# Performance work log

Hardware: AMD Instinct MI355X
Metric: run time of the kernel (lower is better)

Reference implementation:

```python
import jax, jax.numpy as jnp
import numpy as np

N_AGENTS = 32
UNIT_DIM = 64
HIDDEN = 128
BATCH = 1024
STATE_DIM = 128


def setup_inputs() -> dict:
    key = jax.random.key(0)
    ks = jax.random.split(key, 8)
    s = 0.05
    return {
        "state": jax.random.normal(ks[0], (BATCH, STATE_DIM), dtype=jnp.float32),
        "unit_states": jax.random.normal(ks[1], (N_AGENTS, BATCH, UNIT_DIM), dtype=jnp.float32),
        # edge_predictor params, stored [in, out] so y = x @ W + b (matches torch Linear math)
        "W1": jax.random.normal(ks[2], (2 * UNIT_DIM, HIDDEN), dtype=jnp.float32) * s,
        "b1": jnp.zeros((HIDDEN,), dtype=jnp.float32),
        "W2": jax.random.normal(ks[3], (HIDDEN, HIDDEN), dtype=jnp.float32) * s,
        "b2": jnp.zeros((HIDDEN,), dtype=jnp.float32),
        "W3": jax.random.normal(ks[4], (HIDDEN, 1), dtype=jnp.float32) * s,
        "b3": jnp.zeros((1,), dtype=jnp.float32),
    }


def reference(state, unit_states, W1, b1, W2, b2, W3, b3):
    # unit_states: [n_agents, B, d] -> [B, n_agents, d]  (permute(1,0,2))
    us = jnp.transpose(unit_states, (1, 0, 2))
    d = us.shape[-1]
    # Pairwise concat [us_i, us_j] through the first Linear is equivalent to
    # splitting W1 into its i-half and j-half and broadcast-adding (same math,
    # avoids materializing the [B,n,n,2d] concat tensor). Dropout rate is 0.0
    # (eval-mode identity).
    hi = us @ W1[:d]   # [B, n, H]
    hj = us @ W1[d:]   # [B, n, H]
    h = jax.nn.relu(hi[:, :, None, :] + hj[:, None, :, :] + b1)  # [B, n, n, H]
    h = jax.nn.relu(h @ W2 + b2)                                  # [B, n, n, H]
    logits = (h @ W3 + b3)[..., 0]                                # [B, n, n]
    adj = jax.nn.sigmoid(logits)
    # graph_add_self_loop = True
    adj = adj + jnp.eye(adj.shape[-1], dtype=adj.dtype)[None]
    return adj
```

## Files before the change

kernel.cpp:

```cpp
#include <hip/hip_runtime.h>
#include <hip/hip_bf16.h>

#define BATCH 1024
#define NA 32
#define UD 64
#define HID 128

typedef short bf16x8 __attribute__((ext_vector_type(8)));
typedef float f32x4 __attribute__((ext_vector_type(4)));

static __device__ __forceinline__ short f2bf(float x) {
    union { __hip_bfloat16 b; short s; } u;
    u.b = __float2bfloat16(x);
    return u.s;
}

__global__ void prep_weights(const float* __restrict__ W1,
                             const float* __restrict__ W2,
                             short* __restrict__ ws)
{
    int tid  = blockIdx.x * blockDim.x + threadIdx.x;
    int unit = tid >> 6;
    int lane = tid & 63;
    int l15  = lane & 15;
    int lq   = lane >> 4;
    bf16x8 v;
    if (unit < 32) {
        int ks = unit >> 3, nt = unit & 7;
        int col = nt * 16 + l15;
        int k0  = ks * 32 + lq * 8;
        #pragma unroll
        for (int e = 0; e < 8; ++e)
            v[e] = f2bf(W2[(k0 + e) * HID + col]);
    } else {
        int u = unit - 32;
        int h = u >> 4, ks = (u >> 3) & 1, nt = u & 7;
        int col = nt * 16 + l15;
        int k0  = ks * 32 + lq * 8;
        #pragma unroll
        for (int e = 0; e < 8; ++e)
            v[e] = f2bf(W1[(h * UD + k0 + e) * HID + col]);
    }
    *(bf16x8*)&ws[(size_t)(unit * 64 + lane) * 8] = v;
}

template <bool FROM_WS>
__global__ __launch_bounds__(512, 2)
void graph_learner_kernel(const float* __restrict__ us_g,
                          const float* __restrict__ W1,
                          const float* __restrict__ b1,
                          const float* __restrict__ W2,
                          const float* __restrict__ b2,
                          const float* __restrict__ W3,
                          const float* __restrict__ b3,
                          const short* __restrict__ ws,
                          float* __restrict__ out)
{
    __shared__ short us_bf[NA * UD] __attribute__((aligned(16)));
    __shared__ float hi_lds[NA * HID] __attribute__((aligned(16)));
    __shared__ float hj_lds[NA * HID] __attribute__((aligned(16)));

    const int b    = blockIdx.x;
    const int t    = threadIdx.x;
    const int w    = t >> 6;
    const int lane = t & 63;
    const int l15  = lane & 15;
    const int lq   = lane >> 4;

    {
        int i  = t >> 4;
        int d0 = (t & 15) * 4;
        const float* src = us_g + ((size_t)i * BATCH + (size_t)b) * UD + d0;
        float4 v = *(const float4*)src;
        int c  = d0 >> 3;
        int hs = (d0 >> 2) & 1;
        int idx = i * UD + (((c ^ (i & 7)) << 3) + (hs << 2));
        short4 s4;
        s4.x = f2bf(v.x); s4.y = f2bf(v.y); s4.z = f2bf(v.z); s4.w = f2bf(v.w);
        *(short4*)&us_bf[idx] = s4;
    }

    const int Mt  = w >> 2;
    const int nt0 = (w & 3) * 2;

    bf16x8 w1f[2][2][2];
    float  b1v[2];
    bf16x8 w2f[32];
    float  b2v[8], w3v[8];

    #pragma unroll
    for (int n = 0; n < 2; ++n)
        b1v[n] = b1[(nt0 + n) * 16 + l15];
    #pragma unroll
    for (int nt = 0; nt < 8; ++nt) {
        int col = nt * 16 + l15;
        b2v[nt] = b2[col];
        w3v[nt] = W3[col];
    }
    const float b3s = b3[0];

    if (FROM_WS) {
        #pragma unroll
        for (int i = 0; i < 32; ++i)
            w2f[i] = *(const bf16x8*)&ws[(size_t)(i * 64 + lane) * 8];
        #pragma unroll
        for (int n = 0; n < 2; ++n)
            #pragma unroll
            for (int h = 0; h < 2; ++h)
                #pragma unroll
                for (int ks = 0; ks < 2; ++ks) {
                    int u = h * 16 + ks * 8 + (nt0 + n);
                    w1f[n][h][ks] = *(const bf16x8*)&ws[(size_t)((32 + u) * 64 + lane) * 8];
                }
    } else {
        #pragma unroll
        for (int n = 0; n < 2; ++n) {
            int col = (nt0 + n) * 16 + l15;
            #pragma unroll
            for (int ks = 0; ks < 2; ++ks)
                #pragma unroll
                for (int e = 0; e < 8; ++e) {
                    int k = ks * 32 + lq * 8 + e;
                    w1f[n][0][ks][e] = f2bf(W1[k * HID + col]);
                    w1f[n][1][ks][e] = f2bf(W1[(UD + k) * HID + col]);
                }
        }
        #pragma unroll
        for (int ks = 0; ks < 4; ++ks)
            #pragma unroll
            for (int nt = 0; nt < 8; ++nt) {
                int col = nt * 16 + l15;
                int k0  = ks * 32 + lq * 8;
                #pragma unroll
                for (int e = 0; e < 8; ++e)
                    w2f[ks * 8 + nt][e] = f2bf(W2[(k0 + e) * HID + col]);
            }
    }

    __syncthreads();

    {
        const f32x4 zf = {0.f, 0.f, 0.f, 0.f};
        bf16x8 af[2];
        #pragma unroll
        for (int ks = 0; ks < 2; ++ks) {
            int row = Mt * 16 + l15;
            int c   = ks * 4 + lq;
            af[ks] = *(const bf16x8*)&us_bf[row * UD + ((c ^ (row & 7)) << 3)];
        }
        f32x4 ahi[2] = {zf, zf}, ahj[2] = {zf, zf};
        #pragma unroll
        for (int ks = 0; ks < 2; ++ks) {
            #pragma unroll
            for (int n = 0; n < 2; ++n) {
                ahi[n] = __builtin_amdgcn_mfma_f32_16x16x32_bf16(af[ks], w1f[n][0][ks], ahi[n], 0, 0, 0);
                ahj[n] = __builtin_amdgcn_mfma_f32_16x16x32_bf16(af[ks], w1f[n][1][ks], ahj[n], 0, 0, 0);
            }
        }
        #pragma unroll
        for (int n = 0; n < 2; ++n) {
            int col = (nt0 + n) * 16 + l15;
            #pragma unroll
            for (int r = 0; r < 4; ++r) {
                int rowi = Mt * 16 + lq * 4 + r;
                int idx  = rowi * HID + ((((col >> 2) ^ (rowi & 7)) << 2) + (col & 3));
                hi_lds[idx] = ahi[n][r] + b1v[n];
                hj_lds[idx] = ahj[n][r];
            }
        }
    }
    __syncthreads();

    #pragma unroll 1
    for (int mt = w; mt < 64; mt += 8) {
        const int i   = mt >> 1;
        const int j   = ((mt & 1) << 4) + l15;
        const float* hir = &hi_lds[i * HID];
        const float* hjr = &hj_lds[j * HID];
        const int isz = i & 7, jsz = j & 7;

        const f32x4 zf = {0.f, 0.f, 0.f, 0.f};
        f32x4 acc[8];
        #pragma unroll
        for (int nt = 0; nt < 8; ++nt) acc[nt] = zf;

        #pragma unroll
        for (int ks = 0; ks < 4; ++ks) {
            int c0 = ks * 8 + lq * 2;
            f32x4 h0 = *(const f32x4*)&hir[((c0    ) ^ isz) << 2];
            f32x4 h1 = *(const f32x4*)&hir[((c0 + 1) ^ isz) << 2];
            f32x4 g0 = *(const f32x4*)&hjr[((c0    ) ^ jsz) << 2];
            f32x4 g1 = *(const f32x4*)&hjr[((c0 + 1) ^ jsz) << 2];
            bf16x8 a;
            #pragma unroll
            for (int e = 0; e < 4; ++e) {
                a[e]     = f2bf(fmaxf(h0[e] + g0[e], 0.f));
                a[e + 4] = f2bf(fmaxf(h1[e] + g1[e], 0.f));
            }
            #pragma unroll
            for (int nt = 0; nt < 8; ++nt)
                acc[nt] = __builtin_amdgcn_mfma_f32_16x16x32_bf16(a, w2f[ks * 8 + nt], acc[nt], 0, 0, 0);
        }

        float p0r = 0.f, p1r = 0.f, p2r = 0.f, p3r = 0.f;
        #pragma unroll
        for (int nt = 0; nt < 8; ++nt) {
            p0r += fmaxf(acc[nt][0] + b2v[nt], 0.f) * w3v[nt];
            p1r += fmaxf(acc[nt][1] + b2v[nt], 0.f) * w3v[nt];
            p2r += fmaxf(acc[nt][2] + b2v[nt], 0.f) * w3v[nt];
            p3r += fmaxf(acc[nt][3] + b2v[nt], 0.f) * w3v[nt];
        }
        #pragma unroll
        for (int m = 1; m < 16; m <<= 1) {
            p0r += __shfl_xor(p0r, m);
            p1r += __shfl_xor(p1r, m);
            p2r += __shfl_xor(p2r, m);
            p3r += __shfl_xor(p3r, m);
        }
        if (l15 == 0) {
            int pbase = mt * 16 + lq * 4;
            float4 o;
            {
                float x = p0r + b3s; int p = pbase + 0;
                o.x = 1.f / (1.f + __expf(-x)) + (((p >> 5) == (p & 31)) ? 1.f : 0.f);
            }
            {
                float x = p1r + b3s; int p = pbase + 1;
                o.y = 1.f / (1.f + __expf(-x)) + (((p >> 5) == (p & 31)) ? 1.f : 0.f);
            }
            {
                float x = p2r + b3s; int p = pbase + 2;
                o.z = 1.f / (1.f + __expf(-x)) + (((p >> 5) == (p & 31)) ? 1.f : 0.f);
            }
            {
                float x = p3r + b3s; int p = pbase + 3;
                o.w = 1.f / (1.f + __expf(-x)) + (((p >> 5) == (p & 31)) ? 1.f : 0.f);
            }
            *(float4*)&out[(size_t)b * (NA * NA) + pbase] = o;
        }
    }
}

extern "C" void kernel_launch(void* const* d_in, const int* in_sizes, int n_in,
                              void* d_out, int out_size, void* d_ws, size_t ws_size,
                              hipStream_t stream) {
    const float* us = (const float*)d_in[1];
    const float* W1 = (const float*)d_in[2];
    const float* b1 = (const float*)d_in[3];
    const float* W2 = (const float*)d_in[4];
    const float* b2 = (const float*)d_in[5];
    const float* W3 = (const float*)d_in[6];
    const float* b3 = (const float*)d_in[7];
    float* out = (float*)d_out;
    short* ws  = (short*)d_ws;

    const bool use_ws = (ws_size >= 64u * 64u * 8u * sizeof(short));
    if (use_ws) {
        prep_weights<<<dim3(16), dim3(256), 0, stream>>>(W1, W2, ws);
        graph_learner_kernel<true><<<dim3(BATCH), dim3(512), 0, stream>>>(
            us, W1, b1, W2, b2, W3, b3, ws, out);
    } else {
        graph_learner_kernel<false><<<dim3(BATCH), dim3(512), 0, stream>>>(
            us, W1, b1, W2, b2, W3, b3, ws, out);
    }
}
```

Measured before the change: 136.2 us.

## Switch to fp16 MFMA with packed fp16 LDS, transposed layer-2 and 256-thread blocks

Replaces bf16 with fp16 for the weights, unit states and hidden activations. hi/hj are now kept as fp16 in LDS, so the pairwise add and ReLU run as packed half-precision vector ops instead of per-element fp32 math followed by a bf16 convert. The layer-2 MFMA operands are swapped, which puts the output features along lanes; the W3 reduction then needs only two shuffles, and biases are folded into the accumulator initial values. Blocks shrink to 256 threads (4 waves, 16 tiles each) and the W2 register load is deferred until after layer 1. This risks fp16 overflow or precision differences in the hidden sums, and it changes the occupancy balance.

```diff
diff --git a/kernel.cpp b/kernel.cpp
--- a/kernel.cpp
+++ b/kernel.cpp
@@ -6,32 +6,26 @@
 #define UD 64
 #define HID 128
 
-typedef short bf16x8 __attribute__((ext_vector_type(8)));
+typedef _Float16 f16x8 __attribute__((ext_vector_type(8)));
 typedef float f32x4 __attribute__((ext_vector_type(4)));
-
-static __device__ __forceinline__ short f2bf(float x) {
-    union { __hip_bfloat16 b; short s; } u;
-    u.b = __float2bfloat16(x);
-    return u.s;
-}
 
 __global__ void prep_weights(const float* __restrict__ W1,
                              const float* __restrict__ W2,
-                             short* __restrict__ ws)
+                             _Float16* __restrict__ ws)
 {
     int tid  = blockIdx.x * blockDim.x + threadIdx.x;
     int unit = tid >> 6;
     int lane = tid & 63;
     int l15  = lane & 15;
     int lq   = lane >> 4;
-    bf16x8 v;
+    f16x8 v;
     if (unit < 32) {
         int ks = unit >> 3, nt = unit & 7;
         int col = nt * 16 + l15;
         int k0  = ks * 32 + lq * 8;
         #pragma unroll
         for (int e = 0; e < 8; ++e)
-            v[e] = f2bf(W2[(k0 + e) * HID + col]);
+            v[e] = (_Float16)W2[(k0 + e) * HID + col];
     } else {
         int u = unit - 32;
         int h = u >> 4, ks = (u >> 3) & 1, nt = u & 7;
@@ -39,13 +33,13 @@
         int k0  = ks * 32 + lq * 8;
         #pragma unroll
         for (int e = 0; e < 8; ++e)
-            v[e] = f2bf(W1[(h * UD + k0 + e) * HID + col]);
-    }
-    *(bf16x8*)&ws[(size_t)(unit * 64 + lane) * 8] = v;
+            v[e] = (_Float16)W1[(h * UD + k0 + e) * HID + col];
+    }
+    *(f16x8*)&ws[(size_t)(unit * 64 + lane) * 8] = v;
 }
 
 template <bool FROM_WS>
-__global__ __launch_bounds__(512, 2)
+__global__ __launch_bounds__(256, 2)
 void graph_learner_kernel(const float* __restrict__ us_g,
                           const float* __restrict__ W1,
                           const float* __restrict__ b1,
@@ -53,12 +47,12 @@
                           const float* __restrict__ b2,
                           const float* __restrict__ W3,
                           const float* __restrict__ b3,
-                          const short* __restrict__ ws,
+                          const _Float16* __restrict__ ws,
                           float* __restrict__ out)
 {
-    __shared__ short us_bf[NA * UD] __attribute__((aligned(16)));
-    __shared__ float hi_lds[NA * HID] __attribute__((aligned(16)));
-    __shared__ float hj_lds[NA * HID] __attribute__((aligned(16)));
+    __shared__ _Float16 us_f16[NA * UD]  __attribute__((aligned(16)));
+    __shared__ _Float16 hi_lds[NA * HID] __attribute__((aligned(16)));
+    __shared__ _Float16 hj_lds[NA * HID] __attribute__((aligned(16)));
 
     const int b    = blockIdx.x;
     const int t    = threadIdx.x;
@@ -68,63 +62,93 @@
     const int lq   = lane >> 4;
 
     {
-        int i  = t >> 4;
-        int d0 = (t & 15) * 4;
-        const float* src = us_g + ((size_t)i * BATCH + (size_t)b) * UD + d0;
-        float4 v = *(const float4*)src;
-        int c  = d0 >> 3;
-        int hs = (d0 >> 2) & 1;
-        int idx = i * UD + (((c ^ (i & 7)) << 3) + (hs << 2));
-        short4 s4;
-        s4.x = f2bf(v.x); s4.y = f2bf(v.y); s4.z = f2bf(v.z); s4.w = f2bf(v.w);
-        *(short4*)&us_bf[idx] = s4;
-    }
-
-    const int Mt  = w >> 2;
-    const int nt0 = (w & 3) * 2;
-
-    bf16x8 w1f[2][2][2];
-    float  b1v[2];
-    bf16x8 w2f[32];
-    float  b2v[8], w3v[8];
-
-    #pragma unroll
-    for (int n = 0; n < 2; ++n)
-        b1v[n] = b1[(nt0 + n) * 16 + l15];
+        int i  = t >> 3;
+        int c  = t & 7;
+        const float* src = us_g + ((size_t)i * BATCH + (size_t)b) * UD + c * 8;
+        float4 va = *(const float4*)src;
+        float4 vb = *(const float4*)(src + 4);
+        f16x8 v8;
+        v8[0] = (_Float16)va.x; v8[1] = (_Float16)va.y;
+        v8[2] = (_Float16)va.z; v8[3] = (_Float16)va.w;
+        v8[4] = (_Float16)vb.x; v8[5] = (_Float16)vb.y;
+        v8[6] = (_Float16)vb.z; v8[7] = (_Float16)vb.w;
+        *(f16x8*)&us_f16[i * UD + ((c ^ (i & 7)) << 3)] = v8;
+    }
+
+    f32x4 b2q[8], w3q[8];
     #pragma unroll
     for (int nt = 0; nt < 8; ++nt) {
-        int col = nt * 16 + l15;
-        b2v[nt] = b2[col];
-        w3v[nt] = W3[col];
+        b2q[nt] = *(const f32x4*)&b2[nt * 16 + lq * 4];
+        w3q[nt] = *(const f32x4*)&W3[nt * 16 + lq * 4];
     }
     const float b3s = b3[0];
 
-    if (FROM_WS) {
-        #pragma unroll
-        for (int i = 0; i < 32; ++i)
-            w2f[i] = *(const bf16x8*)&ws[(size_t)(i * 64 + lane) * 8];
-        #pragma unroll
-        for (int n = 0; n < 2; ++n)
+    const int Mt = w >> 1;
+    const int nh = w & 1;
+
+    f16x8 w1f[4][2][2];
+    float b1v[4];
+    #pragma unroll
+    for (int n = 0; n < 4; ++n) {
+        int nt = nh * 4 + n;
+        b1v[n] = b1[nt * 16 + l15];
+        if (FROM_WS) {
             #pragma unroll
             for (int h = 0; h < 2; ++h)
                 #pragma unroll
                 for (int ks = 0; ks < 2; ++ks) {
-                    int u = h * 16 + ks * 8 + (nt0 + n);
-                    w1f[n][h][ks] = *(const bf16x8*)&ws[(size_t)((32 + u) * 64 + lane) * 8];
+                    int u = 32 + h * 16 + ks * 8 + nt;
+                    w1f[n][h][ks] = *(const f16x8*)&ws[(size_t)(u * 64 + lane) * 8];
                 }
+        } else {
+            int col = nt * 16 + l15;
+            #pragma unroll
+            for (int h = 0; h < 2; ++h)
+                #pragma unroll
+                for (int ks = 0; ks < 2; ++ks)
+                    #pragma unroll
+                    for (int e = 0; e < 8; ++e)
+                        w1f[n][h][ks][e] = (_Float16)W1[(h * UD + ks * 32 + lq * 8 + e) * HID + col];
+        }
+    }
+
+    __syncthreads();
+
+    {
+        f16x8 af[2];
+        #pragma unroll
+        for (int ks = 0; ks < 2; ++ks) {
+            int row = Mt * 16 + l15;
+            int c   = ks * 4 + lq;
+            af[ks] = *(const f16x8*)&us_f16[row * UD + ((c ^ (row & 7)) << 3)];
+        }
+        #pragma unroll
+        for (int n = 0; n < 4; ++n) {
+            int nt = nh * 4 + n;
+            f32x4 ahi = {b1v[n], b1v[n], b1v[n], b1v[n]};
+            f32x4 ahj = {0.f, 0.f, 0.f, 0.f};
+            #pragma unroll
+            for (int ks = 0; ks < 2; ++ks) {
+                ahi = __builtin_amdgcn_mfma_f32_16x16x32_f16(af[ks], w1f[n][0][ks], ahi, 0, 0, 0);
+                ahj = __builtin_amdgcn_mfma_f32_16x16x32_f16(af[ks], w1f[n][1][ks], ahj, 0, 0, 0);
+            }
+            #pragma unroll
+            for (int r = 0; r < 4; ++r) {
+                int row = Mt * 16 + lq * 4 + r;
+                int col = nt * 16 + l15;
+                int idx = row * HID + ((((col >> 3) ^ (row & 15)) << 3) + (col & 7));
+                hi_lds[idx] = (_Float16)ahi[r];
+                hj_lds[idx] = (_Float16)ahj[r];
+            }
+        }
+    }
+
+    f16x8 w2f[32];
+    if (FROM_WS) {
+        #pragma unroll
+        for (int q = 0; q < 32; ++q)
+            w2f[q] = *(const f16x8*)&ws[(size_t)(q * 64 + lane) * 8];
     } else {
-        #pragma unroll
-        for (int n = 0; n < 2; ++n) {
-            int col = (nt0 + n) * 16 + l15;
-            #pragma unroll
-            for (int ks = 0; ks < 2; ++ks)
-                #pragma unroll
-                for (int e = 0; e < 8; ++e) {
-                    int k = ks * 32 + lq * 8 + e;
-                    w1f[n][0][ks][e] = f2bf(W1[k * HID + col]);
-                    w1f[n][1][ks][e] = f2bf(W1[(UD + k) * HID + col]);
-                }
-        }
         #pragma unroll
         for (int ks = 0; ks < 4; ++ks)
             #pragma unroll
@@ -133,111 +157,59 @@
                 int k0  = ks * 32 + lq * 8;
                 #pragma unroll
                 for (int e = 0; e < 8; ++e)
-                    w2f[ks * 8 + nt][e] = f2bf(W2[(k0 + e) * HID + col]);
+                    w2f[ks * 8 + nt][e] = (_Float16)W2[(k0 + e) * HID + col];
             }
     }
 
     __syncthreads();
 
-    {
-        const f32x4 zf = {0.f, 0.f, 0.f, 0.f};
-        bf16x8 af[2];
-        #pragma unroll
-        for (int ks = 0; ks < 2; ++ks) {
-            int row = Mt * 16 + l15;
-            int c   = ks * 4 + lq;
-            af[ks] = *(const bf16x8*)&us_bf[row * UD + ((c ^ (row & 7)) << 3)];
-        }
-        f32x4 ahi[2] = {zf, zf}, ahj[2] = {zf, zf};
-        #pragma unroll
-        for (int ks = 0; ks < 2; ++ks) {
-            #pragma unroll
-            for (int n = 0; n < 2; ++n) {
-                ahi[n] = __builtin_amdgcn_mfma_f32_16x16x32_bf16(af[ks], w1f[n][0][ks], ahi[n], 0, 0, 0);
-                ahj[n] = __builtin_amdgcn_mfma_f32_16x16x32_bf16(af[ks], w1f[n][1][ks], ahj[n], 0, 0, 0);
-            }
-        }
-        #pragma unroll
-        for (int n = 0; n < 2; ++n) {
-            int col = (nt0 + n) * 16 + l15;
-            #pragma unroll
-            for (int r = 0; r < 4; ++r) {
-                int rowi = Mt * 16 + lq * 4 + r;
-                int idx  = rowi * HID + ((((col >> 2) ^ (rowi & 7)) << 2) + (col & 3));
-                hi_lds[idx] = ahi[n][r] + b1v[n];
-                hj_lds[idx] = ahj[n][r];
-            }
-        }
-    }
-    __syncthreads();
+    #pragma unroll
+    for (int q = 0; q < 32; q += 4)
+        asm volatile("" : "+v"(w2f[q]), "+v"(w2f[q + 1]), "+v"(w2f[q + 2]), "+v"(w2f[q + 3]));
 
     #pragma unroll 1
-    for (int mt = w; mt < 64; mt += 8) {
-        const int i   = mt >> 1;
-        const int j   = ((mt & 1) << 4) + l15;
-        const float* hir = &hi_lds[i * HID];
-        const float* hjr = &hj_lds[j * HID];
-        const int isz = i & 7, jsz = j & 7;
-
-        const f32x4 zf = {0.f, 0.f, 0.f, 0.f};
+    for (int tt = 0; tt < 16; ++tt) {
+        const int mt = w + tt * 4;
+        const int i  = mt >> 1;
+        const int j  = ((mt & 1) << 4) + l15;
+        const _Float16* hir = &hi_lds[i * HID];
+        const _Float16* hjr = &hj_lds[j * HID];
+        const int isz = i & 15, jsz = j & 15;
+
         f32x4 acc[8];
         #pragma unroll
-        for (int nt = 0; nt < 8; ++nt) acc[nt] = zf;
+        for (int nt = 0; nt < 8; ++nt) acc[nt] = b2q[nt];
 
         #pragma unroll
         for (int ks = 0; ks < 4; ++ks) {
-            int c0 = ks * 8 + lq * 2;
-            f32x4 h0 = *(const f32x4*)&hir[((c0    ) ^ isz) << 2];
-            f32x4 h1 = *(const f32x4*)&hir[((c0 + 1) ^ isz) << 2];
-            f32x4 g0 = *(const f32x4*)&hjr[((c0    ) ^ jsz) << 2];
-            f32x4 g1 = *(const f32x4*)&hjr[((c0 + 1) ^ jsz) << 2];
-            bf16x8 a;
-            #pragma unroll
-            for (int e = 0; e < 4; ++e) {
-                a[e]     = f2bf(fmaxf(h0[e] + g0[e], 0.f));
-                a[e + 4] = f2bf(fmaxf(h1[e] + g1[e], 0.f));
-            }
+            int c0 = ks * 4 + lq;
+            f16x8 hi8 = *(const f16x8*)&hir[(c0 ^ isz) << 3];
+            f16x8 hj8 = *(const f16x8*)&hjr[(c0 ^ jsz) << 3];
+            f16x8 s   = hi8 + hj8;
+            f16x8 z   = {};
+            f16x8 xb  = __builtin_elementwise_max(s, z);
             #pragma unroll
             for (int nt = 0; nt < 8; ++nt)
-                acc[nt] = __builtin_amdgcn_mfma_f32_16x16x32_bf16(a, w2f[ks * 8 + nt], acc[nt], 0, 0, 0);
-        }
-
-        float p0r = 0.f, p1r = 0.f, p2r = 0.f, p3r = 0.f;
+                acc[nt] = __builtin_amdgcn_mfma_f32_16x16x32_f16(w2f[ks * 8 + nt], xb, acc[nt], 0, 0, 0);
+        }
+
+        float p = 0.f;
         #pragma unroll
         for (int nt = 0; nt < 8; ++nt) {
-            p0r += fmaxf(acc[nt][0] + b2v[nt], 0.f) * w3v[nt];
-            p1r += fmaxf(acc[nt][1] + b2v[nt], 0.f) * w3v[nt];
-            p2r += fmaxf(acc[nt][2] + b2v[nt], 0.f) * w3v[nt];
-            p3r += fmaxf(acc[nt][3] + b2v[nt], 0.f) * w3v[nt];
-        }
-        #pragma unroll
-        for (int m = 1; m < 16; m <<= 1) {
-            p0r += __shfl_xor(p0r, m);
-            p1r += __shfl_xor(p1r, m);
-            p2r += __shfl_xor(p2r, m);
-            p3r += __shfl_xor(p3r, m);
-        }
-        if (l15 == 0) {
-            int pbase = mt * 16 + lq * 4;
-            float4 o;
-            {
-                float x = p0r + b3s; int p = pbase + 0;
-                o.x = 1.f / (1.f + __expf(-x)) + (((p >> 5) == (p & 31)) ? 1.f : 0.f);
-            }
-            {
-                float x = p1r + b3s; int p = pbase + 1;
-                o.y = 1.f / (1.f + __expf(-x)) + (((p >> 5) == (p & 31)) ? 1.f : 0.f);
-            }
-            {
-                float x = p2r + b3s; int p = pbase + 2;
-                o.z = 1.f / (1.f + __expf(-x)) + (((p >> 5) == (p & 31)) ? 1.f : 0.f);
-            }
-            {
-                float x = p3r + b3s; int p = pbase + 3;
-                o.w = 1.f / (1.f + __expf(-x)) + (((p >> 5) == (p & 31)) ? 1.f : 0.f);
-            }
-            *(float4*)&out[(size_t)b * (NA * NA) + pbase] = o;
-        }
+            p += fmaxf(acc[nt][0], 0.f) * w3q[nt][0];
+            p += fmaxf(acc[nt][1], 0.f) * w3q[nt][1];
+            p += fmaxf(acc[nt][2], 0.f) * w3q[nt][2];
+            p += fmaxf(acc[nt][3], 0.f) * w3q[nt][3];
+        }
+        p += __shfl_xor(p, 16);
+        p += __shfl_xor(p, 32);
+
+        float x  = p + b3s;
+        float sg = 1.f / (1.f + __expf(-x));
+        int   pi = mt * 16 + l15;
+        sg += ((pi >> 5) == (pi & 31)) ? 1.f : 0.f;
+        if (lane < 16)
+            out[(size_t)b * (NA * NA) + pi] = sg;
     }
 }
 
@@ -252,15 +224,15 @@
     const float* W3 = (const float*)d_in[6];
     const float* b3 = (const float*)d_in[7];
     float* out = (float*)d_out;
-    short* ws  = (short*)d_ws;
-
-    const bool use_ws = (ws_size >= 64u * 64u * 8u * sizeof(short));
+    _Float16* ws = (_Float16*)d_ws;
+
+    const bool use_ws = (ws_size >= 64u * 64u * 8u * sizeof(_Float16));
     if (use_ws) {
         prep_weights<<<dim3(16), dim3(256), 0, stream>>>(W1, W2, ws);
-        graph_learner_kernel<true><<<dim3(BATCH), dim3(512), 0, stream>>>(
+        graph_learner_kernel<true><<<dim3(BATCH), dim3(256), 0, stream>>>(
             us, W1, b1, W2, b2, W3, b3, ws, out);
     } else {
-        graph_learner_kernel<false><<<dim3(BATCH), dim3(512), 0, stream>>>(
+        graph_learner_kernel<false><<<dim3(BATCH), dim3(256), 0, stream>>>(
             us, W1, b1, W2, b2, W3, b3, ws, out);
     }
 }
```

After: 116.1 us. 14.7% less time.
